# Kernel tuning notes

Measured on AMD Instinct MI355X. Metric: run time of the kernel, lower is better.

The kernel has to match this reference:

```python
import jax, jax.numpy as jnp
import numpy as np

N = 50000   # nodes
E = 600000  # edges
H = 128     # hidden_dim


def _linear_params(key, fan_in, fan_out):
    kw, kb = jax.random.split(key)
    s = 1.0 / np.sqrt(fan_in)
    w = jax.random.uniform(kw, (fan_in, fan_out), minval=-s, maxval=s, dtype=jnp.float32)
    b = jax.random.uniform(kb, (fan_out,), minval=-s, maxval=s, dtype=jnp.float32)
    return w, b


def setup_inputs():
    key = jax.random.key(0)
    ks = jax.random.split(key, 9)
    x = jax.random.uniform(ks[0], (N, 1), dtype=jnp.float32)
    pre_h = jax.random.normal(ks[1], (N, H), dtype=jnp.float32)
    edge_index = jax.random.randint(ks[2], (2, E), 0, N, dtype=jnp.int32)
    edge_attr = jax.random.uniform(ks[3], (E, 1), dtype=jnp.float32)
    enc_w, enc_b = _linear_params(ks[4], 1 + H, H)      # BFS_Encoder.linear
    M_w, M_b = _linear_params(ks[5], H + H + 1, H)      # MPNN_Processor.M
    U_w, U_b = _linear_params(ks[6], H + H, H)          # MPNN_Processor.U
    dec_w, dec_b = _linear_params(ks[7], H + H, 1)      # BFS_Decoder.linear
    ter_w, ter_b = _linear_params(ks[8], H + H, 1)      # BFS_Terminator.linear
    return {"x": x, "pre_h": pre_h, "edge_attr": edge_attr,
            "enc_w": enc_w, "enc_b": enc_b, "M_w": M_w, "M_b": M_b,
            "U_w": U_w, "U_b": U_b, "dec_w": dec_w, "dec_b": dec_b,
            "ter_w": ter_w, "ter_b": ter_b, "edge_index": edge_index}


def reference(x, pre_h, edge_attr, enc_w, enc_b, M_w, M_b, U_w, U_b,
              dec_w, dec_b, ter_w, ter_b, edge_index):
    # Encoder: z = relu(Linear([x, pre_h]))
    z = jax.nn.relu(jnp.concatenate([x, pre_h], axis=-1) @ enc_w + enc_b)  # [N,H]

    # Processor (PyG MessagePassing, flow source_to_target):
    # z_i = z[edge_index[1]] (target), z_j = z[edge_index[0]] (source)
    src, tgt = edge_index[0], edge_index[1]
    m = jax.nn.relu(
        jnp.concatenate([z[tgt], z[src], edge_attr], axis=-1) @ M_w + M_b)  # [E,H]
    # scatter-max aggregate into target nodes; empty segments -> 0
    agg = jax.ops.segment_max(m, tgt, num_segments=N)
    agg = jnp.where(jnp.isfinite(agg), agg, 0.0)
    h = jax.nn.relu(jnp.concatenate([z, agg], axis=-1) @ U_w + U_b)  # [N,H]

    # Decoder
    y = jax.nn.sigmoid(jnp.concatenate([z, h], axis=-1) @ dec_w + dec_b)  # [N,1]

    # Terminator: mean over nodes, broadcast-concat, scalar mean
    h_mean = jnp.broadcast_to(jnp.mean(h, axis=0), h.shape)
    ter = jnp.mean(jnp.concatenate([h, h_mean], axis=-1) @ ter_w + ter_b)
    return h, y, ter
```

## Files before the change

kernel.cpp:

```cpp
#include <hip/hip_runtime.h>
#include <hip/hip_bf16.h>
#include <math.h>

#define HD 128
#define APAD 136

typedef short bf16x8 __attribute__((ext_vector_type(8)));
typedef float f32x4 __attribute__((ext_vector_type(4)));

static __device__ __forceinline__ unsigned short f2bf(float f) {
  __hip_bfloat16 b = __float2bfloat16(f);
  return *(unsigned short*)&b;
}
static __device__ __forceinline__ float bflo(unsigned int u) {
  return __uint_as_float(u << 16);
}
static __device__ __forceinline__ float bfhi(unsigned int u) {
  return __uint_as_float(u & 0xffff0000u);
}

__global__ __launch_bounds__(256) void k_frag_hist(
    const float* __restrict__ enc_w, const float* __restrict__ M_w,
    const float* __restrict__ U_w,
    unsigned short* __restrict__ encf, unsigned short* __restrict__ Pf,
    unsigned short* __restrict__ Qf, unsigned short* __restrict__ Uf,
    const int* __restrict__ ei, int* __restrict__ cnt,
    int* __restrict__ eoff, int E) {
  const int b = blockIdx.x;
  if (b >= 40) {
    const int e = (b - 40) * 256 + threadIdx.x;
    if (e < E) eoff[e] = atomicAdd(&cnt[ei[E + e]], 1);
    return;
  }
  const float* W; unsigned short* F; int KS; int lb;
  if (b < 8)       { W = enc_w + HD;     F = encf; KS = 4; lb = b; }
  else if (b < 16) { W = M_w;            F = Pf;   KS = 4; lb = b - 8; }
  else if (b < 24) { W = M_w + HD * HD;  F = Qf;   KS = 4; lb = b - 16; }
  else             { W = U_w;            F = Uf;   KS = 8; lb = b - 24; }
  const int gid = lb * 256 + threadIdx.x;
  const int lane = gid & 63;
  const int ks = (gid >> 6) % KS;
  const int tile = gid / (64 * KS);
  const int col = tile * 16 + (lane & 15);
  const int k0 = ks * 32 + (lane >> 4) * 8;
  unsigned short v[8];
#pragma unroll
  for (int j = 0; j < 8; ++j) v[j] = f2bf(W[(size_t)(k0 + j) * HD + col]);
  unsigned short* dst = F + ((size_t)(tile * KS + ks) * 64 + lane) * 8;
#pragma unroll
  for (int j = 0; j < 8; ++j) dst[j] = v[j];
}

__global__ __launch_bounds__(256) void k_scan1(
    int* __restrict__ cursor, int* __restrict__ row_ptr,
    unsigned long long* __restrict__ flags, int N) {
  __shared__ int s[256];
  __shared__ int poff_sh;
  const int t = threadIdx.x, b = blockIdx.x;
  const int base = b * 1024 + t * 4;
  int v[4], sum = 0;
#pragma unroll
  for (int i = 0; i < 4; ++i) {
    v[i] = (base + i < N) ? cursor[base + i] : 0;
    sum += v[i];
  }
  s[t] = sum;
  __syncthreads();
  for (int off = 1; off < 256; off <<= 1) {
    int xv = (t >= off) ? s[t - off] : 0;
    __syncthreads();
    if (t >= off) s[t] += xv;
    __syncthreads();
  }
  if (t == 0)
    atomicExch(&flags[b], ((unsigned long long)(unsigned)s[255] << 32) | 1ull);
  if (t < 64) {
    int acc = 0;
    if (t < b) {
      unsigned long long f;
      do { f = atomicAdd(&flags[t], 0ull); } while (!(f & 1ull));
      acc = (int)(f >> 32);
    }
#pragma unroll
    for (int o = 32; o > 0; o >>= 1) acc += __shfl_down(acc, o);
    if (t == 0) poff_sh = acc;
  }
  __syncthreads();
  int run = s[t] - sum + poff_sh;
#pragma unroll
  for (int i = 0; i < 4; ++i) {
    if (base + i < N) {
      row_ptr[base + i] = run;
      cursor[base + i]  = run + v[i];
      run += v[i];
    }
  }
}

__global__ __launch_bounds__(256, 4) void k_scatter_enc(
    const int* __restrict__ ei, const float* __restrict__ edge_attr,
    const int* __restrict__ row_ptr, const int* __restrict__ eoff,
    int2* __restrict__ epack, int E, int eb,
    const float* __restrict__ x, const float* __restrict__ pre_h,
    const float* __restrict__ enc_w, const float* __restrict__ enc_b,
    const float* __restrict__ M_b,
    const unsigned short* __restrict__ encf, const unsigned short* __restrict__ Pf,
    const unsigned short* __restrict__ Qf,
    unsigned short* __restrict__ zg, unsigned short* __restrict__ Pg,
    unsigned short* __restrict__ Qg) {
  __shared__ unsigned short phs[16 * APAD];
  __shared__ unsigned short zsh[16 * APAD];
  __shared__ float xs[16];
  const int t = threadIdx.x;

  if (blockIdx.x < (unsigned)eb) {
    const int e = blockIdx.x * 256 + t;
    if (e < E) {
      const int tgt = ei[E + e];
      const int pos = row_ptr[tgt] + eoff[e];
      epack[pos] = make_int2(ei[e], __float_as_int(edge_attr[e]));
    }
    return;
  }

  const int n0 = (blockIdx.x - eb) * 16;
  {
    const int r = t >> 4, c0 = (t & 15) * 8;
    const float4 a = *(const float4*)&pre_h[(size_t)(n0 + r) * HD + c0];
    const float4 b = *(const float4*)&pre_h[(size_t)(n0 + r) * HD + c0 + 4];
    unsigned short* d = &phs[r * APAD + c0];
    d[0] = f2bf(a.x); d[1] = f2bf(a.y); d[2] = f2bf(a.z); d[3] = f2bf(a.w);
    d[4] = f2bf(b.x); d[5] = f2bf(b.y); d[6] = f2bf(b.z); d[7] = f2bf(b.w);
  }
  if (t < 16) xs[t] = x[n0 + t];
  __syncthreads();

  const int w = t >> 6, l = t & 63;
  const int m = l & 15, q = l >> 4;

  bf16x8 af[4];
#pragma unroll
  for (int ks = 0; ks < 4; ++ks)
    af[ks] = *(const bf16x8*)&phs[m * APAD + ks * 32 + q * 8];
  f32x4 acc[2] = {{0, 0, 0, 0}, {0, 0, 0, 0}};
#pragma unroll
  for (int tt = 0; tt < 2; ++tt) {
    const int tn = 2 * w + tt;
#pragma unroll
    for (int ks = 0; ks < 4; ++ks) {
      const bf16x8 bf = *(const bf16x8*)&encf[((size_t)(tn * 4 + ks) * 64 + l) * 8];
      acc[tt] = __builtin_amdgcn_mfma_f32_16x16x32_bf16(af[ks], bf, acc[tt], 0, 0, 0);
    }
  }
#pragma unroll
  for (int tt = 0; tt < 2; ++tt) {
    const int col = (2 * w + tt) * 16 + m;
    const float bb = enc_b[col];
    const float w0 = enc_w[col];
#pragma unroll
    for (int r = 0; r < 4; ++r) {
      const int row = q * 4 + r;
      const float zv = fmaxf(acc[tt][r] + bb + xs[row] * w0, 0.0f);
      zsh[row * APAD + col] = f2bf(zv);
    }
  }
  __syncthreads();

  bf16x8 az[4];
#pragma unroll
  for (int ks = 0; ks < 4; ++ks)
    az[ks] = *(const bf16x8*)&zsh[m * APAD + ks * 32 + q * 8];
  {
    const int r = t >> 4, c0 = (t & 15) * 8;
    *(uint4*)&zg[(size_t)(n0 + r) * HD + c0] = *(const uint4*)&zsh[r * APAD + c0];
  }
  __syncthreads();

  f32x4 pacc[2] = {{0, 0, 0, 0}, {0, 0, 0, 0}};
  f32x4 qacc[2] = {{0, 0, 0, 0}, {0, 0, 0, 0}};
#pragma unroll
  for (int tt = 0; tt < 2; ++tt) {
    const int tn = 2 * w + tt;
#pragma unroll
    for (int ks = 0; ks < 4; ++ks) {
      const bf16x8 bp = *(const bf16x8*)&Pf[((size_t)(tn * 4 + ks) * 64 + l) * 8];
      const bf16x8 bq = *(const bf16x8*)&Qf[((size_t)(tn * 4 + ks) * 64 + l) * 8];
      pacc[tt] = __builtin_amdgcn_mfma_f32_16x16x32_bf16(az[ks], bp, pacc[tt], 0, 0, 0);
      qacc[tt] = __builtin_amdgcn_mfma_f32_16x16x32_bf16(az[ks], bq, qacc[tt], 0, 0, 0);
    }
  }
#pragma unroll
  for (int tt = 0; tt < 2; ++tt) {
    const int col = (2 * w + tt) * 16 + m;
    const float mb = M_b[col];
#pragma unroll
    for (int r = 0; r < 4; ++r) {
      const int row = q * 4 + r;
      phs[row * APAD + col] = f2bf(pacc[tt][r] + mb);
      zsh[row * APAD + col] = f2bf(qacc[tt][r]);
    }
  }
  __syncthreads();
  {
    const int r = t >> 4, c0 = (t & 15) * 8;
    *(uint4*)&Pg[(size_t)(n0 + r) * HD + c0] = *(const uint4*)&phs[r * APAD + c0];
    *(uint4*)&Qg[(size_t)(n0 + r) * HD + c0] = *(const uint4*)&zsh[r * APAD + c0];
  }
}

__global__ __launch_bounds__(256, 4) void k_gu(
    const unsigned short* __restrict__ zg, const unsigned short* __restrict__ Pg,
    const unsigned short* __restrict__ Qg, const float* __restrict__ w_attr,
    const int* __restrict__ row_ptr, const int* __restrict__ row_end,
    const int2* __restrict__ epack, const unsigned short* __restrict__ Uf,
    const float* __restrict__ U_b, const float* __restrict__ dec_w,
    const float* __restrict__ dec_b,
    float* __restrict__ h_out, float* __restrict__ y_out,
    float* __restrict__ hpart, int N) {
  __shared__ unsigned short zsh[32 * APAD];
  __shared__ unsigned short ash[32 * APAD];
  __shared__ float hcol[HD];
  __shared__ float dacc[32];
  __shared__ float pr[32][8];
  const int t = threadIdx.x;
  const int n0 = blockIdx.x * 32;

  {
    const int r = t >> 3, c0 = (t & 7) * 16;
    const int n = min(n0 + r, N - 1);
    *(uint4*)&zsh[r * APAD + c0]     = *(const uint4*)&zg[(size_t)n * HD + c0];
    *(uint4*)&zsh[r * APAD + c0 + 8] = *(const uint4*)&zg[(size_t)n * HD + c0 + 8];
  }
  if (t < 32) dacc[t] = 0.0f;
  if (t < HD) hcol[t] = 0.0f;

  const int w = t >> 6, l = t & 63;
  const int g = l >> 4, j = l & 15;

  float wv[8];
  {
    const float4 wa = *(const float4*)&w_attr[j * 8];
    const float4 wb = *(const float4*)&w_attr[j * 8 + 4];
    wv[0] = wa.x; wv[1] = wa.y; wv[2] = wa.z; wv[3] = wa.w;
    wv[4] = wb.x; wv[5] = wb.y; wv[6] = wb.z; wv[7] = wb.w;
  }
  {
    const int r0 = w * 8 + g * 2, r1 = r0 + 1;
    const int nn0 = n0 + r0, nn1 = n0 + r1;
    const int rs0 = row_ptr[min(nn0, N - 1)], re0 = row_end[min(nn0, N - 1)];
    const int rs1 = row_ptr[min(nn1, N - 1)], re1 = row_end[min(nn1, N - 1)];
    const bool v0 = re0 > rs0, v1 = re1 > rs1;
    float ac0[8], ac1[8];
#pragma unroll
    for (int c = 0; c < 8; ++c) { ac0[c] = -INFINITY; ac1[c] = -INFINITY; }
    const int nb0 = v0 ? ((re0 - rs0 + 7) >> 3) : 0;
    const int nb1 = v1 ? ((re1 - rs1 + 7) >> 3) : 0;
    const int nbat = max(nb0, nb1);
    int e0 = rs0, e1 = rs1;
    for (int b = 0; b < nbat; ++b) {
      int2 pk0[8], pk1[8];
#pragma unroll
      for (int u = 0; u < 8; ++u) {
        pk0[u] = epack[v0 ? min(e0 + u, re0 - 1) : 0];
        pk1[u] = epack[v1 ? min(e1 + u, re1 - 1) : 0];
      }
      uint4 qv0[8], qv1[8];
#pragma unroll
      for (int u = 0; u < 8; ++u)
        qv0[u] = *(const uint4*)&Qg[(size_t)pk0[u].x * HD + j * 8];
#pragma unroll
      for (int u = 0; u < 8; ++u)
        qv1[u] = *(const uint4*)&Qg[(size_t)pk1[u].x * HD + j * 8];
#pragma unroll
      for (int u = 0; u < 8; ++u) {
        const float a = __int_as_float(pk0[u].y);
        const unsigned int qq[4] = {qv0[u].x, qv0[u].y, qv0[u].z, qv0[u].w};
#pragma unroll
        for (int c = 0; c < 4; ++c) {
          ac0[2 * c]     = fmaxf(ac0[2 * c],     fmaf(a, wv[2 * c],     bflo(qq[c])));
          ac0[2 * c + 1] = fmaxf(ac0[2 * c + 1], fmaf(a, wv[2 * c + 1], bfhi(qq[c])));
        }
      }
#pragma unroll
      for (int u = 0; u < 8; ++u) {
        const float a = __int_as_float(pk1[u].y);
        const unsigned int qq[4] = {qv1[u].x, qv1[u].y, qv1[u].z, qv1[u].w};
#pragma unroll
        for (int c = 0; c < 4; ++c) {
          ac1[2 * c]     = fmaxf(ac1[2 * c],     fmaf(a, wv[2 * c],     bflo(qq[c])));
          ac1[2 * c + 1] = fmaxf(ac1[2 * c + 1], fmaf(a, wv[2 * c + 1], bfhi(qq[c])));
        }
      }
      e0 += 8; e1 += 8;
    }
    {
      float res[8];
      if (nn0 < N && v0) {
        const uint4 pv = *(const uint4*)&Pg[(size_t)nn0 * HD + j * 8];
        const unsigned int pp[4] = {pv.x, pv.y, pv.z, pv.w};
#pragma unroll
        for (int c = 0; c < 4; ++c) {
          res[2 * c]     = fmaxf(bflo(pp[c]) + ac0[2 * c],     0.0f);
          res[2 * c + 1] = fmaxf(bfhi(pp[c]) + ac0[2 * c + 1], 0.0f);
        }
      } else {
#pragma unroll
        for (int c = 0; c < 8; ++c) res[c] = 0.0f;
      }
      uint4 st;
      st.x = (unsigned)f2bf(res[0]) | ((unsigned)f2bf(res[1]) << 16);
      st.y = (unsigned)f2bf(res[2]) | ((unsigned)f2bf(res[3]) << 16);
      st.z = (unsigned)f2bf(res[4]) | ((unsigned)f2bf(res[5]) << 16);
      st.w = (unsigned)f2bf(res[6]) | ((unsigned)f2bf(res[7]) << 16);
      *(uint4*)&ash[r0 * APAD + j * 8] = st;
    }
    {
      float res[8];
      if (nn1 < N && v1) {
        const uint4 pv = *(const uint4*)&Pg[(size_t)nn1 * HD + j * 8];
        const unsigned int pp[4] = {pv.x, pv.y, pv.z, pv.w};
#pragma unroll
        for (int c = 0; c < 4; ++c) {
          res[2 * c]     = fmaxf(bflo(pp[c]) + ac1[2 * c],     0.0f);
          res[2 * c + 1] = fmaxf(bfhi(pp[c]) + ac1[2 * c + 1], 0.0f);
        }
      } else {
#pragma unroll
        for (int c = 0; c < 8; ++c) res[c] = 0.0f;
      }
      uint4 st;
      st.x = (unsigned)f2bf(res[0]) | ((unsigned)f2bf(res[1]) << 16);
      st.y = (unsigned)f2bf(res[2]) | ((unsigned)f2bf(res[3]) << 16);
      st.z = (unsigned)f2bf(res[4]) | ((unsigned)f2bf(res[5]) << 16);
      st.w = (unsigned)f2bf(res[6]) | ((unsigned)f2bf(res[7]) << 16);
      *(uint4*)&ash[r1 * APAD + j * 8] = st;
    }
  }
  __syncthreads();

  const int mt = w & 1, nh = w >> 1;
  const int m = mt * 16 + (l & 15), q = l >> 4;
  bf16x8 afz[4], afa[4];
#pragma unroll
  for (int ks = 0; ks < 4; ++ks) {
    afz[ks] = *(const bf16x8*)&zsh[m * APAD + ks * 32 + q * 8];
    afa[ks] = *(const bf16x8*)&ash[m * APAD + ks * 32 + q * 8];
  }
  f32x4 acc4[4] = {{0, 0, 0, 0}, {0, 0, 0, 0}, {0, 0, 0, 0}, {0, 0, 0, 0}};
#pragma unroll
  for (int tt = 0; tt < 4; ++tt) {
    const int tn = nh * 4 + tt;
#pragma unroll
    for (int ks = 0; ks < 8; ++ks) {
      const bf16x8 bf = *(const bf16x8*)&Uf[((size_t)(tn * 8 + ks) * 64 + l) * 8];
      const bf16x8 a = (ks < 4) ? afz[ks] : afa[ks - 4];
      acc4[tt] = __builtin_amdgcn_mfma_f32_16x16x32_bf16(a, bf, acc4[tt], 0, 0, 0);
    }
  }
  float dp[4] = {0.0f, 0.0f, 0.0f, 0.0f};
#pragma unroll
  for (int tt = 0; tt < 4; ++tt) {
    const int col = (nh * 4 + tt) * 16 + (l & 15);
    const float ub = U_b[col];
    const float dw = dec_w[HD + col];
    float s4 = 0.0f;
#pragma unroll
    for (int r = 0; r < 4; ++r) {
      const int rowl = mt * 16 + q * 4 + r;
      const int n = n0 + rowl;
      float hv = fmaxf(acc4[tt][r] + ub, 0.0f);
      if (n < N) h_out[(size_t)n * HD + col] = hv; else hv = 0.0f;
      s4 += hv;
      dp[r] += hv * dw;
    }
    atomicAdd(&hcol[col], s4);
  }
#pragma unroll
  for (int off = 1; off < 16; off <<= 1) {
#pragma unroll
    for (int r = 0; r < 4; ++r) dp[r] += __shfl_xor(dp[r], off);
  }
  if ((l & 15) == 0) {
#pragma unroll
    for (int r = 0; r < 4; ++r) atomicAdd(&dacc[mt * 16 + q * 4 + r], dp[r]);
  }
  {
    const int r2 = t >> 3, s = t & 7;
    float part = 0.0f;
#pragma unroll
    for (int c = 0; c < 8; ++c) {
      const int kk = s * 16 + 2 * c;
      const unsigned int zu = *(const unsigned int*)&zsh[r2 * APAD + kk];
      part += bflo(zu) * dec_w[kk] + bfhi(zu) * dec_w[kk + 1];
    }
    pr[r2][s] = part;
  }
  __syncthreads();

  if (t < HD) hpart[(size_t)blockIdx.x * HD + t] = hcol[t];
  if (t < 32 && n0 + t < N) {
    float d = dec_b[0] + dacc[t];
#pragma unroll
    for (int s = 0; s < 8; ++s) d += pr[t][s];
    y_out[n0 + t] = 1.0f / (1.0f + expf(-d));
  }
}

__global__ __launch_bounds__(256) void k_hred_ter(
    const float* __restrict__ hpart, float* __restrict__ hsum,
    int* __restrict__ done,
    const float* __restrict__ ter_w, const float* __restrict__ ter_b,
    float* __restrict__ out, float invN, int NB, int nblk) {
  __shared__ float sh[HD];
  __shared__ float r2[2];
  __shared__ int last;
  const int t = threadIdx.x;
  const int col = t & (HD - 1);
  const int half = t >> 7;
  float acc = 0.0f;
  for (int r = blockIdx.x * 2 + half; r < NB; r += nblk * 2)
    acc += hpart[(size_t)r * HD + col];
  if (half) sh[col] = acc;
  __syncthreads();
  if (!half) atomicAdd(&hsum[col], acc + sh[col]);
  __threadfence();
  __syncthreads();
  if (t == 0) last = (atomicAdd(done, 1) == nblk - 1);
  __syncthreads();
  if (!last) return;
  float v = 0.0f;
  if (t < HD) {
    const float cs = atomicAdd(&hsum[t], 0.0f);
    v = (cs * invN) * (ter_w[t] + ter_w[HD + t]);
  }
#pragma unroll
  for (int o = 32; o > 0; o >>= 1) v += __shfl_down(v, o);
  if (t < HD && (t & 63) == 0) r2[t >> 6] = v;
  __syncthreads();
  if (t == 0) out[0] = r2[0] + r2[1] + ter_b[0];
}

extern "C" void kernel_launch(void* const* d_in, const int* in_sizes, int n_in,
                              void* d_out, int out_size, void* d_ws, size_t ws_size,
                              hipStream_t stream) {
  const float* x        = (const float*)d_in[0];
  const float* pre_h    = (const float*)d_in[1];
  const float* edge_attr= (const float*)d_in[2];
  const float* enc_w    = (const float*)d_in[3];
  const float* enc_b    = (const float*)d_in[4];
  const float* M_w      = (const float*)d_in[5];
  const float* M_b      = (const float*)d_in[6];
  const float* U_w      = (const float*)d_in[7];
  const float* U_b      = (const float*)d_in[8];
  const float* dec_w    = (const float*)d_in[9];
  const float* dec_b    = (const float*)d_in[10];
  const float* ter_w    = (const float*)d_in[11];
  const float* ter_b    = (const float*)d_in[12];
  const int*   edge_idx = (const int*)d_in[13];

  const int N = in_sizes[0];
  const int E = in_sizes[2];
  const size_t NH = (size_t)N * HD;

  float* out = (float*)d_out;
  float* h_out = out;
  float* y_out = out + NH;
  float* ter_out = out + NH + N;

  unsigned short* zg = (unsigned short*)d_ws;
  unsigned short* Pg = zg + NH;
  unsigned short* Qg = Pg + NH;
  int*   cursor   = (int*)(Qg + NH);
  unsigned long long* flags = (unsigned long long*)(cursor + N);
  int*   done     = (int*)(flags + 64);
  float* hsum     = (float*)(done + 2);
  int*   row_ptr  = (int*)(hsum + HD);
  int2*  epack    = (int2*)(row_ptr + N);
  int*   eoff     = (int*)(epack + E);
  unsigned short* encf = (unsigned short*)(eoff + E);
  unsigned short* Pf   = encf + 8 * 4 * 64 * 8;
  unsigned short* Qf   = Pf + 8 * 4 * 64 * 8;
  unsigned short* Uf   = Qf + 8 * 4 * 64 * 8;
  float* hpart = (float*)(Uf + 16 * 256 * 8);

  const size_t zero_bytes = (size_t)N * 4 + 64 * 8 + 2 * 4 + HD * 4;
  hipMemsetAsync(cursor, 0, zero_bytes, stream);

  const int scan_blocks = (N + 1023) / 1024;
  const int eb = (E + 255) / 256;
  const int nb32 = (N + 31) / 32;

  k_frag_hist<<<40 + eb, 256, 0, stream>>>(enc_w, M_w, U_w, encf, Pf, Qf, Uf,
                                           edge_idx, cursor, eoff, E);
  k_scan1<<<scan_blocks, 256, 0, stream>>>(cursor, row_ptr, flags, N);
  k_scatter_enc<<<eb + N / 16, 256, 0, stream>>>(
      edge_idx, edge_attr, row_ptr, eoff, epack, E, eb,
      x, pre_h, enc_w, enc_b, M_b, encf, Pf, Qf, zg, Pg, Qg);
  k_gu<<<nb32, 256, 0, stream>>>(
      zg, Pg, Qg, M_w + 256 * HD, row_ptr, cursor, epack, Uf,
      U_b, dec_w, dec_b, h_out, y_out, hpart, N);
  k_hred_ter<<<64, 256, 0, stream>>>(hpart, hsum, done, ter_w, ter_b, ter_out,
                                     1.0f / (float)N, nb32, 64);
}
```

Baseline: 221.8 us.

## Fuse histogram and prefix scan into one kernel via last-blocks ticket

Merges the edge-degree histogram kernel and the exclusive-scan kernel into one launch. Histogram blocks take a ticket from a global counter, and the last scan_blocks finishers spin until all histogram blocks are done, then perform the decoupled scan over the counts. This removes one kernel launch and its inter-kernel gap. It relies on the counter in done[1] being zeroed by the existing memset and on spin-waiting, which adds deadlock and contention risk.

```diff
diff --git a/kernel.cpp b/kernel.cpp
--- a/kernel.cpp
+++ b/kernel.cpp
@@ -19,49 +19,63 @@
   return __uint_as_float(u & 0xffff0000u);
 }
 
-__global__ __launch_bounds__(256) void k_frag_hist(
+__global__ __launch_bounds__(256) void k_frag_hist_scan(
     const float* __restrict__ enc_w, const float* __restrict__ M_w,
     const float* __restrict__ U_w,
     unsigned short* __restrict__ encf, unsigned short* __restrict__ Pf,
     unsigned short* __restrict__ Qf, unsigned short* __restrict__ Uf,
     const int* __restrict__ ei, int* __restrict__ cnt,
-    int* __restrict__ eoff, int E) {
+    int* __restrict__ eoff, int E,
+    int* __restrict__ row_ptr, unsigned long long* __restrict__ flags,
+    int* __restrict__ done, int N, int eb, int scan_blocks) {
   const int b = blockIdx.x;
-  if (b >= 40) {
-    const int e = (b - 40) * 256 + threadIdx.x;
+  const int t = threadIdx.x;
+
+  if (b < 40) {
+    const float* W; unsigned short* F; int KS; int lb;
+    if (b < 8)       { W = enc_w + HD;     F = encf; KS = 4; lb = b; }
+    else if (b < 16) { W = M_w;            F = Pf;   KS = 4; lb = b - 8; }
+    else if (b < 24) { W = M_w + HD * HD;  F = Qf;   KS = 4; lb = b - 16; }
+    else             { W = U_w;            F = Uf;   KS = 8; lb = b - 24; }
+    const int gid = lb * 256 + t;
+    const int lane = gid & 63;
+    const int ks = (gid >> 6) % KS;
+    const int tile = gid / (64 * KS);
+    const int col = tile * 16 + (lane & 15);
+    const int k0 = ks * 32 + (lane >> 4) * 8;
+    unsigned short v[8];
+#pragma unroll
+    for (int j = 0; j < 8; ++j) v[j] = f2bf(W[(size_t)(k0 + j) * HD + col]);
+    unsigned short* dst = F + ((size_t)(tile * KS + ks) * 64 + lane) * 8;
+#pragma unroll
+    for (int j = 0; j < 8; ++j) dst[j] = v[j];
+    return;
+  }
+
+  {
+    const int e = (b - 40) * 256 + t;
     if (e < E) eoff[e] = atomicAdd(&cnt[ei[E + e]], 1);
-    return;
-  }
-  const float* W; unsigned short* F; int KS; int lb;
-  if (b < 8)       { W = enc_w + HD;     F = encf; KS = 4; lb = b; }
-  else if (b < 16) { W = M_w;            F = Pf;   KS = 4; lb = b - 8; }
-  else if (b < 24) { W = M_w + HD * HD;  F = Qf;   KS = 4; lb = b - 16; }
-  else             { W = U_w;            F = Uf;   KS = 8; lb = b - 24; }
-  const int gid = lb * 256 + threadIdx.x;
-  const int lane = gid & 63;
-  const int ks = (gid >> 6) % KS;
-  const int tile = gid / (64 * KS);
-  const int col = tile * 16 + (lane & 15);
-  const int k0 = ks * 32 + (lane >> 4) * 8;
-  unsigned short v[8];
-#pragma unroll
-  for (int j = 0; j < 8; ++j) v[j] = f2bf(W[(size_t)(k0 + j) * HD + col]);
-  unsigned short* dst = F + ((size_t)(tile * KS + ks) * 64 + lane) * 8;
-#pragma unroll
-  for (int j = 0; j < 8; ++j) dst[j] = v[j];
-}
-
-__global__ __launch_bounds__(256) void k_scan1(
-    int* __restrict__ cursor, int* __restrict__ row_ptr,
-    unsigned long long* __restrict__ flags, int N) {
+  }
+  __shared__ int ticket_sh;
+  __syncthreads();
+  __threadfence();
+  if (t == 0) ticket_sh = atomicAdd(&done[1], 1);
+  __syncthreads();
+  const int sb = ticket_sh - (eb - scan_blocks);
+  if (sb < 0) return;
+
+  if (t == 0) {
+    while (atomicAdd(&done[1], 0) < eb) { }
+  }
+  __syncthreads();
+
   __shared__ int s[256];
   __shared__ int poff_sh;
-  const int t = threadIdx.x, b = blockIdx.x;
-  const int base = b * 1024 + t * 4;
+  const int base = sb * 1024 + t * 4;
   int v[4], sum = 0;
 #pragma unroll
   for (int i = 0; i < 4; ++i) {
-    v[i] = (base + i < N) ? cursor[base + i] : 0;
+    v[i] = (base + i < N) ? atomicAdd(&cnt[base + i], 0) : 0;
     sum += v[i];
   }
   s[t] = sum;
@@ -73,10 +87,10 @@
     __syncthreads();
   }
   if (t == 0)
-    atomicExch(&flags[b], ((unsigned long long)(unsigned)s[255] << 32) | 1ull);
+    atomicExch(&flags[sb], ((unsigned long long)(unsigned)s[255] << 32) | 1ull);
   if (t < 64) {
     int acc = 0;
-    if (t < b) {
+    if (t < sb) {
       unsigned long long f;
       do { f = atomicAdd(&flags[t], 0ull); } while (!(f & 1ull));
       acc = (int)(f >> 32);
@@ -91,7 +105,7 @@
   for (int i = 0; i < 4; ++i) {
     if (base + i < N) {
       row_ptr[base + i] = run;
-      cursor[base + i]  = run + v[i];
+      cnt[base + i]     = run + v[i];
       run += v[i];
     }
   }
@@ -490,9 +504,10 @@
   const int eb = (E + 255) / 256;
   const int nb32 = (N + 31) / 32;
 
-  k_frag_hist<<<40 + eb, 256, 0, stream>>>(enc_w, M_w, U_w, encf, Pf, Qf, Uf,
-                                           edge_idx, cursor, eoff, E);
-  k_scan1<<<scan_blocks, 256, 0, stream>>>(cursor, row_ptr, flags, N);
+  k_frag_hist_scan<<<40 + eb, 256, 0, stream>>>(
+      enc_w, M_w, U_w, encf, Pf, Qf, Uf,
+      edge_idx, cursor, eoff, E,
+      row_ptr, flags, done, N, eb, scan_blocks);
   k_scatter_enc<<<eb + N / 16, 256, 0, stream>>>(
       edge_idx, edge_attr, row_ptr, eoff, epack, E, eb,
       x, pre_h, enc_w, enc_b, M_b, encf, Pf, Qf, zg, Pg, Qg);
```

Result: slower. 369.0 us (+66.4%).
